# Optimization experiments

Hardware: AMD Instinct MI355X
Metric: run time of the kernel (lower is better)

Reference implementation:

```python
import jax, jax.numpy as jnp
import numpy as np


def segment_softmax(x, seg, num_segments):
    # numerically-stable softmax over graph segments (rows of the sparse matrix)
    m = jax.ops.segment_max(x, seg, num_segments=num_segments)
    e = jnp.exp(x - m[seg])
    s = jax.ops.segment_sum(e, seg, num_segments=num_segments)
    return e / s[seg]


def setup_inputs() -> dict:
    key = jax.random.key(0)
    ks = jax.random.split(key, 12)
    B, N, E, P, H = 256, 51200, 102400, 5, 300
    instruction = jax.random.normal(ks[0], (B, H), dtype=jnp.float32)
    distribution = jax.random.uniform(ks[1], (N,), dtype=jnp.float32)
    node_attrs = jax.random.normal(ks[2], (N, H), dtype=jnp.float32)
    edge_attrs = jax.random.normal(ks[3], (E, H), dtype=jnp.float32)
    node_indices = jnp.sort(jax.random.randint(ks[4], (N,), 0, B)).astype(jnp.int32)
    edge_batch_indices = jax.random.randint(ks[5], (E,), 0, B).astype(jnp.int32)
    edge_indices = jax.random.randint(ks[6], (2, E), 0, N).astype(jnp.int32)
    prop_embeds = jax.random.normal(ks[7], (P, H), dtype=jnp.float32)
    Ws_property = jax.random.uniform(ks[8], (P, H, H), dtype=jnp.float32)
    W_state = jax.random.uniform(ks[9], (H,), dtype=jnp.float32)
    W_relation = jax.random.uniform(ks[10], (H,), dtype=jnp.float32)
    return {"instruction": instruction, "distribution": distribution, "node_attrs": node_attrs,
            "edge_attrs": edge_attrs, "node_indices": node_indices,
            "edge_batch_indices": edge_batch_indices, "edge_indices": edge_indices,
            "prop_embeds": prop_embeds, "Ws_property": Ws_property,
            "W_state": W_state, "W_relation": W_relation}


def reference(instruction, distribution, node_attrs, edge_attrs, node_indices,
              edge_batch_indices, edge_indices, prop_embeds, Ws_property,
              W_state, W_relation):
    B = instruction.shape[0]
    # [B, P] property similarities
    prop_sim = jax.nn.softmax(instruction @ prop_embeds.T, axis=1)
    ps_node = prop_sim[node_indices]            # [N, P]
    instr_node = instruction[node_indices]      # [N, H]
    # per-property transform of node attrs: [N, P-1, H]
    wx = jnp.einsum('phk,nk->nph', Ws_property[:-1], node_attrs)
    node_scores = jax.nn.elu(jnp.sum(ps_node[:, :-1, None] * instr_node[:, None, :] * wx, axis=1))  # [N, H]
    # relation transform of edge attrs: [E, H]
    edge_wx = jnp.einsum('hk,ek->eh', Ws_property[-1], edge_attrs)
    edge_scores = jax.nn.elu(instruction[edge_batch_indices] * edge_wx)  # [E, H]
    # per-graph (segment) softmax over state logits
    state_logits = node_scores @ W_state        # [N]
    next_states = segment_softmax(state_logits, node_indices, B)
    # scatter-add message passing: dst node accumulates distribution[src] * edge_scores
    agg = jnp.zeros_like(node_scores).at[edge_indices[1]].add(
        distribution[edge_indices[0], None] * edge_scores)  # [N, H]
    rel_logits = agg @ W_relation               # [N]
    next_relations = segment_softmax(rel_logits, node_indices, B)
    r = ps_node[:, -1]
    next_distribution = r * next_relations + (1.0 - r) * next_states
    return next_distribution, prop_sim
```

## Files before the change

kernel.cpp:

```cpp
#include <hip/hip_runtime.h>
#include <math.h>

#define H 300
#define PP 5
#define NE 128
#define KC 32
#define NCH 10
#define WROWS 320
#define ROWB 128
#define WTILE (WROWS * ROWB)
#define ATILE (NE * ROWB)
#define NTHREADS 256
#define GT 512

using short8 = __attribute__((ext_vector_type(8))) short;
using f32x4  = __attribute__((ext_vector_type(4))) float;

__device__ __forceinline__ float wsum64(float v) {
#pragma unroll
    for (int m = 32; m >= 1; m >>= 1) v += __shfl_xor(v, m, 64);
    return v;
}
__device__ __forceinline__ float wmax64(float v) {
#pragma unroll
    for (int m = 32; m >= 1; m >>= 1) v = fmaxf(v, __shfl_xor(v, m, 64));
    return v;
}
__device__ __forceinline__ float eluf(float x) { return x > 0.f ? x : expm1f(x); }

__device__ __forceinline__ unsigned short f2bf(float x) {
    unsigned int u = __float_as_uint(x);
    unsigned int r = u + 0x7FFF + ((u >> 16) & 1);
    return (unsigned short)(r >> 16);
}
__device__ __forceinline__ float bf2f(unsigned short h) {
    return __uint_as_float(((unsigned int)h) << 16);
}
__device__ __forceinline__ int sw(int r, int kb) {
    return r * ROWB + (kb ^ ((r & 7) << 4));
}
__device__ __forceinline__ void split4(const float* v, uint2& ph, uint2& pl) {
    unsigned short hs[4], ls[4];
#pragma unroll
    for (int i = 0; i < 4; ++i) {
        hs[i] = f2bf(v[i]);
        ls[i] = f2bf(v[i] - bf2f(hs[i]));
    }
    ph = make_uint2((unsigned)hs[0] | ((unsigned)hs[1] << 16),
                    (unsigned)hs[2] | ((unsigned)hs[3] << 16));
    pl = make_uint2((unsigned)ls[0] | ((unsigned)ls[1] << 16),
                    (unsigned)ls[2] | ((unsigned)ls[3] << 16));
}
__device__ __forceinline__ void gload16(const void* g, void* lds) {
    __builtin_amdgcn_global_load_lds(
        (const __attribute__((address_space(1))) unsigned int*)g,
        (__attribute__((address_space(3))) unsigned int*)lds, 16, 0, 0);
}
#define SBAR() __builtin_amdgcn_s_barrier()
#define SCHED() __builtin_amdgcn_sched_barrier(0)
#define WAIT_LGKM() asm volatile("s_waitcnt lgkmcnt(0)" ::: "memory")
#define WAIT_VM2()  asm volatile("s_waitcnt vmcnt(2) lgkmcnt(0)" ::: "memory")
#define WAIT_VM0()  asm volatile("s_waitcnt vmcnt(0) lgkmcnt(0)" ::: "memory")

__global__ void k_prop_sim(const float* __restrict__ instr,
                           const float* __restrict__ pe,
                           float* __restrict__ prop_sim) {
    int b = blockIdx.x, lane = threadIdx.x;
    float dots[PP];
#pragma unroll
    for (int p = 0; p < PP; ++p) {
        float s = 0.f;
        for (int hh = lane; hh < H; hh += 64) s += instr[b * H + hh] * pe[p * H + hh];
        dots[p] = wsum64(s);
    }
    if (lane == 0) {
        float m = dots[0];
#pragma unroll
        for (int p = 1; p < PP; ++p) m = fmaxf(m, dots[p]);
        float e[PP], s = 0.f;
#pragma unroll
        for (int p = 0; p < PP; ++p) { e[p] = expf(dots[p] - m); s += e[p]; }
        float inv = 1.f / s;
#pragma unroll
        for (int p = 0; p < PP; ++p) prop_sim[b * PP + p] = e[p] * inv;
    }
}

__global__ void k_counts(const int* __restrict__ idx, int* __restrict__ counts, int N) {
    int i = blockIdx.x * blockDim.x + threadIdx.x;
    if (i < N) atomicAdd(&counts[idx[i]], 1);
}

__global__ void k_scan(const int* __restrict__ counts, int* __restrict__ offsets, int B) {
    __shared__ int sh[256];
    int t = threadIdx.x;
    int c = (t < B) ? counts[t] : 0;
    sh[t] = c;
    __syncthreads();
    for (int off = 1; off < 256; off <<= 1) {
        int v = (t >= off) ? sh[t - off] : 0;
        __syncthreads();
        sh[t] += v;
        __syncthreads();
    }
    if (t < B) offsets[t] = sh[t] - c;
    if (t == B - 1) offsets[B] = sh[t];
}

__global__ void k_presplit(const float* __restrict__ W4, char* __restrict__ img) {
    int c = blockIdx.x;
    int idx = blockIdx.y * NTHREADS + threadIdx.x;
    int r = idx >> 3, j = idx & 7;
    int k = c * KC + j * 4;
    float v[4] = {0.f, 0.f, 0.f, 0.f};
    if (r < H && k < H) *(float4*)v = *(const float4*)&W4[(size_t)r * H + k];
    uint2 ph, pl;
    split4(v, ph, pl);
    char* row = img + (size_t)c * WTILE + (size_t)r * ROWB;
    int x = (r & 7) << 4;
    *(uint2*)(row + ((j * 8) ^ x)) = ph;
    *(uint2*)(row + ((64 + j * 8) ^ x)) = pl;
}

__global__ void k_combine(const float* __restrict__ Ws,
                          const float* __restrict__ prop_sim,
                          char* __restrict__ img) {
    int b = blockIdx.x, c = blockIdx.y, t = threadIdx.x;
    float ps0 = prop_sim[b * PP + 0], ps1 = prop_sim[b * PP + 1];
    float ps2 = prop_sim[b * PP + 2], ps3 = prop_sim[b * PP + 3];
    char* tile = img + ((size_t)b * NCH + c) * WTILE;
#pragma unroll
    for (int i = 0; i < 10; ++i) {
        int idx = t + i * NTHREADS;
        int r = idx >> 3, j = idx & 7;
        int k = c * KC + j * 4;
        float cv[4] = {0.f, 0.f, 0.f, 0.f};
        if (r < H && k < H) {
            size_t base = (size_t)r * H + k;
            float w0[4], w1[4], w2[4], w3[4];
            *(float4*)w0 = *(const float4*)&Ws[0 * (size_t)H * H + base];
            *(float4*)w1 = *(const float4*)&Ws[1 * (size_t)H * H + base];
            *(float4*)w2 = *(const float4*)&Ws[2 * (size_t)H * H + base];
            *(float4*)w3 = *(const float4*)&Ws[3 * (size_t)H * H + base];
#pragma unroll
            for (int q = 0; q < 4; ++q)
                cv[q] = fmaf(ps0, w0[q], fmaf(ps1, w1[q], fmaf(ps2, w2[q], ps3 * w3[q])));
        }
        uint2 ph, pl;
        split4(cv, ph, pl);
        char* row = tile + (size_t)r * ROWB;
        int x = (r & 7) << 4;
        *(uint2*)(row + ((j * 8) ^ x)) = ph;
        *(uint2*)(row + ((64 + j * 8) ^ x)) = pl;
    }
}

__global__ __launch_bounds__(GT, 2) void k_gemm(
    const float* __restrict__ na, const float* __restrict__ ea,
    const char* __restrict__ Wc_img, const char* __restrict__ Wr_img,
    const float* __restrict__ instr, const float* __restrict__ wstate,
    const float* __restrict__ wrel,
    const int* __restrict__ offsets, const int* __restrict__ eb,
    const int* __restrict__ ei, const float* __restrict__ dist,
    float* __restrict__ slog, float* __restrict__ rlog,
    int N, int E, int nodeBlks)
{
    __shared__ __align__(16) char W_t[WTILE];
    __shared__ __align__(16) char A_t[ATILE];

    int bid = blockIdx.x;
    bool isNode = bid < nodeBlks;
    const float* Asrc;
    const char* Wsrc;
    int base, rowmax, b = 0, nn = NE;
    if (isNode) {
        int low3 = bid & 7, q = bid >> 3;
        int tile = q % 3, bhi = q / 3;
        b = bhi * 8 + low3;
        int start = offsets[b], end = offsets[b + 1];
        base = start + tile * NE;
        if (base >= end) return;
        nn = min(NE, end - base);
        rowmax = N - 1;
        Asrc = na;
        Wsrc = Wc_img + (size_t)b * NCH * WTILE;
    } else {
        base = (bid - nodeBlks) * NE;
        rowmax = E - 1;
        Asrc = ea;
        Wsrc = Wr_img;
    }

    int t = threadIdx.x;
    int w = t >> 6, l = t & 63, lane16 = l & 15, g = l >> 4;
    int wn = w & 3, wh = w >> 2;

    f32x4 acc[10][2];
#pragma unroll
    for (int ht = 0; ht < 10; ++ht)
#pragma unroll
        for (int cg = 0; cg < 2; ++cg) acc[ht][cg] = (f32x4){0.f, 0.f, 0.f, 0.f};

    float4 pa[2];
    auto loadA = [&](int c) {
#pragma unroll
        for (int i = 0; i < 2; ++i) {
            int idx = t + i * GT;
            int r = idx >> 3, j = idx & 7;
            int k = c * KC + j * 4;
            float4 v = {0.f, 0.f, 0.f, 0.f};
            if (k < H) {
                int row = min(base + r, rowmax);
                v = *(const float4*)&Asrc[(size_t)row * H + k];
            }
            pa[i] = v;
        }
    };
    auto storeA = [&]() {
#pragma unroll
        for (int i = 0; i < 2; ++i) {
            int idx = t + i * GT;
            int r = idx >> 3, j = idx & 7;
            float v[4] = {pa[i].x, pa[i].y, pa[i].z, pa[i].w};
            uint2 ph, pl;
            split4(v, ph, pl);
            *(uint2*)(A_t + sw(r, j * 8)) = ph;
            *(uint2*)(A_t + sw(r, 64 + j * 8)) = pl;
        }
    };
    auto gloadW = [&](int c) {
        const char* src = Wsrc + (size_t)c * WTILE;
        int goff = w * 5120 + (t & 63) * 16;
        int loff = w * 5120;
#pragma unroll
        for (int s = 0; s < 5; ++s)
            gload16(src + s * 1024 + goff, W_t + s * 1024 + loff);
    };

    loadA(0);
    storeA();
    gloadW(0);
    SCHED();
    loadA(1);
    SCHED();
    WAIT_VM2();
    SBAR();
    SCHED();

    for (int c = 0; c < NCH; ++c) {
        short8 bh[2], bl[2];
#pragma unroll
        for (int cg = 0; cg < 2; ++cg) {
            int brow = wn * 32 + cg * 16 + lane16;
            bh[cg] = *(const short8*)(A_t + sw(brow, g * 16));
            bl[cg] = *(const short8*)(A_t + sw(brow, 64 + g * 16));
        }
#pragma unroll
        for (int ht = 0; ht < 10; ++ht) {
            int arow = (wh * 10 + ht) * 16 + lane16;
            short8 ah = *(const short8*)(W_t + sw(arow, g * 16));
            short8 al = *(const short8*)(W_t + sw(arow, 64 + g * 16));
#pragma unroll
            for (int cg = 0; cg < 2; ++cg) {
                acc[ht][cg] = __builtin_amdgcn_mfma_f32_16x16x32_bf16(ah, bh[cg], acc[ht][cg], 0, 0, 0);
                acc[ht][cg] = __builtin_amdgcn_mfma_f32_16x16x32_bf16(ah, bl[cg], acc[ht][cg], 0, 0, 0);
                acc[ht][cg] = __builtin_amdgcn_mfma_f32_16x16x32_bf16(al, bh[cg], acc[ht][cg], 0, 0, 0);
            }
        }
        if (c + 1 < NCH) {
            WAIT_LGKM();
            SBAR();
            SCHED();
            storeA();
            gloadW(c + 1);
            SCHED();
            if (c + 2 < NCH) {
                loadA(c + 2);
                SCHED();
                WAIT_VM2();
            } else {
                WAIT_VM0();
            }
            SBAR();
            SCHED();
        }
    }

    if (isNode) {
        const float* insb = instr + (size_t)b * H;
#pragma unroll
        for (int cg = 0; cg < 2; ++cg) {
            float part = 0.f;
#pragma unroll
            for (int ht = 0; ht < 10; ++ht) {
                int hb = wh * 160 + ht * 16 + g * 4;
#pragma unroll
                for (int r = 0; r < 4; ++r) {
                    int h = hb + r;
                    if (h < H) part += wstate[h] * eluf(insb[h] * acc[ht][cg][r]);
                }
            }
            part += __shfl_xor(part, 16, 64);
            part += __shfl_xor(part, 32, 64);
            int col = wn * 32 + cg * 16 + lane16;
            if (l < 16 && col < nn) atomicAdd(&slog[base + col], part);
        }
    } else {
#pragma unroll
        for (int cg = 0; cg < 2; ++cg) {
            int e = base + wn * 32 + cg * 16 + lane16;
            int be = eb[e];
            const float* insb = instr + (size_t)be * H;
            float part = 0.f;
#pragma unroll
            for (int ht = 0; ht < 10; ++ht) {
                int hb = wh * 160 + ht * 16 + g * 4;
#pragma unroll
                for (int r = 0; r < 4; ++r) {
                    int h = hb + r;
                    if (h < H) part += wrel[h] * eluf(insb[h] * acc[ht][cg][r]);
                }
            }
            part += __shfl_xor(part, 16, 64);
            part += __shfl_xor(part, 32, 64);
            if (l < 16) atomicAdd(&rlog[ei[E + e]], dist[ei[e]] * part);
        }
    }
}

__global__ void k_final(const float* __restrict__ slog, const float* __restrict__ rlog,
                        const float* __restrict__ prop_sim, const int* __restrict__ offsets,
                        float* __restrict__ out)
{
    int b = blockIdx.x;
    int s0 = offsets[b], e1 = offsets[b + 1];
    int t = threadIdx.x, wave = t >> 6, lane = t & 63;
    __shared__ float shA[4], shB[4];
    float mS = -3.0e38f, mR = -3.0e38f;
    for (int i = s0 + t; i < e1; i += 256) {
        mS = fmaxf(mS, slog[i]);
        mR = fmaxf(mR, rlog[i]);
    }
    mS = wmax64(mS); mR = wmax64(mR);
    if (lane == 0) { shA[wave] = mS; shB[wave] = mR; }
    __syncthreads();
    mS = fmaxf(fmaxf(shA[0], shA[1]), fmaxf(shA[2], shA[3]));
    mR = fmaxf(fmaxf(shB[0], shB[1]), fmaxf(shB[2], shB[3]));
    __syncthreads();
    float sS = 0.f, sR = 0.f;
    for (int i = s0 + t; i < e1; i += 256) {
        sS += expf(slog[i] - mS);
        sR += expf(rlog[i] - mR);
    }
    sS = wsum64(sS); sR = wsum64(sR);
    if (lane == 0) { shA[wave] = sS; shB[wave] = sR; }
    __syncthreads();
    sS = shA[0] + shA[1] + shA[2] + shA[3];
    sR = shB[0] + shB[1] + shB[2] + shB[3];
    float r = prop_sim[b * PP + (PP - 1)];
    float iS = 1.f / sS, iR = 1.f / sR;
    for (int i = s0 + t; i < e1; i += 256) {
        float ns = expf(slog[i] - mS) * iS;
        float nr = expf(rlog[i] - mR) * iR;
        out[i] = r * nr + (1.f - r) * ns;
    }
}

extern "C" void kernel_launch(void* const* d_in, const int* in_sizes, int n_in,
                              void* d_out, int out_size, void* d_ws, size_t ws_size,
                              hipStream_t stream) {
    (void)n_in; (void)out_size; (void)ws_size;
    const float* instruction  = (const float*)d_in[0];
    const float* distribution = (const float*)d_in[1];
    const float* node_attrs   = (const float*)d_in[2];
    const float* edge_attrs   = (const float*)d_in[3];
    const int*   node_indices = (const int*)d_in[4];
    const int*   edge_batch   = (const int*)d_in[5];
    const int*   edge_indices = (const int*)d_in[6];
    const float* prop_embeds  = (const float*)d_in[7];
    const float* Ws           = (const float*)d_in[8];
    const float* W_state      = (const float*)d_in[9];
    const float* W_rel        = (const float*)d_in[10];

    int B = in_sizes[0] / H;
    int N = in_sizes[1];
    int E = in_sizes[5];

    float* out = (float*)d_out;
    float* prop_sim = out + N;

    float* ws = (float*)d_ws;
    float* state_logits = ws;
    float* rel_logits   = ws + N;
    int*   offsets      = (int*)(ws + 2 * (size_t)N);
    int*   counts       = offsets + (B + 1);
    uintptr_t wsp = (uintptr_t)(counts + B);
    wsp = (wsp + 255) & ~(uintptr_t)255;
    char* Wr_img = (char*)wsp;
    char* Wc_img = Wr_img + (size_t)NCH * WTILE;

    size_t zero_bytes = (size_t)2 * N * sizeof(float) + (size_t)(2 * B + 1) * sizeof(int);
    hipMemsetAsync(d_ws, 0, zero_bytes, stream);

    int nodeBlks = 3 * B;
    int edgeBlks = E / NE;

    k_prop_sim<<<B, 64, 0, stream>>>(instruction, prop_embeds, prop_sim);
    k_presplit<<<dim3(NCH, 10), NTHREADS, 0, stream>>>(Ws + 4 * (size_t)H * H, Wr_img);
    k_counts<<<(N + 255) / 256, 256, 0, stream>>>(node_indices, counts, N);
    k_scan<<<1, 256, 0, stream>>>(counts, offsets, B);
    k_combine<<<dim3(B, NCH), NTHREADS, 0, stream>>>(Ws, prop_sim, Wc_img);
    k_gemm<<<nodeBlks + edgeBlks, GT, 0, stream>>>(
        node_attrs, edge_attrs, Wc_img, Wr_img, instruction, W_state, W_rel,
        offsets, edge_batch, edge_indices, distribution,
        state_logits, rel_logits, N, E, nodeBlks);
    k_final<<<B, 256, 0, stream>>>(state_logits, rel_logits, prop_sim, offsets, out);
}
```

Before: 367.5 us.

## Rebalance wave tiling to 4x2 and stage W through registers instead of direct LDS loads

Each wave now covers 80 output rows by 64 columns (5x4 MFMA tiles) instead of 160x32, so each A fragment read from LDS feeds more MFMAs and fewer W fragment reads are needed per chunk. The W tile is no longer loaded with global_load_lds; it is prefetched into registers and written to LDS alongside the A tile, and the wait before the barrier becomes an lgkmcnt wait. This trades LDS read traffic and the direct-to-LDS path for extra VGPR pressure and explicit register staging of W, which could lower occupancy.

```diff
diff --git a/kernel.cpp b/kernel.cpp
--- a/kernel.cpp
+++ b/kernel.cpp
@@ -51,16 +51,9 @@
     pl = make_uint2((unsigned)ls[0] | ((unsigned)ls[1] << 16),
                     (unsigned)ls[2] | ((unsigned)ls[3] << 16));
 }
-__device__ __forceinline__ void gload16(const void* g, void* lds) {
-    __builtin_amdgcn_global_load_lds(
-        (const __attribute__((address_space(1))) unsigned int*)g,
-        (__attribute__((address_space(3))) unsigned int*)lds, 16, 0, 0);
-}
 #define SBAR() __builtin_amdgcn_s_barrier()
 #define SCHED() __builtin_amdgcn_sched_barrier(0)
 #define WAIT_LGKM() asm volatile("s_waitcnt lgkmcnt(0)" ::: "memory")
-#define WAIT_VM2()  asm volatile("s_waitcnt vmcnt(2) lgkmcnt(0)" ::: "memory")
-#define WAIT_VM0()  asm volatile("s_waitcnt vmcnt(0) lgkmcnt(0)" ::: "memory")
 
 __global__ void k_prop_sim(const float* __restrict__ instr,
                            const float* __restrict__ pe,
@@ -193,15 +186,17 @@
 
     int t = threadIdx.x;
     int w = t >> 6, l = t & 63, lane16 = l & 15, g = l >> 4;
-    int wn = w & 3, wh = w >> 2;
-
-    f32x4 acc[10][2];
-#pragma unroll
-    for (int ht = 0; ht < 10; ++ht)
-#pragma unroll
-        for (int cg = 0; cg < 2; ++cg) acc[ht][cg] = (f32x4){0.f, 0.f, 0.f, 0.f};
+    int wn = w & 1, wh = w >> 1;
+
+    f32x4 acc[5][4];
+#pragma unroll
+    for (int ht = 0; ht < 5; ++ht)
+#pragma unroll
+        for (int cg = 0; cg < 4; ++cg) acc[ht][cg] = (f32x4){0.f, 0.f, 0.f, 0.f};
 
     float4 pa[2];
+    uint4  pw[5];
+
     auto loadA = [&](int c) {
 #pragma unroll
         for (int i = 0; i < 2; ++i) {
@@ -228,40 +223,42 @@
             *(uint2*)(A_t + sw(r, 64 + j * 8)) = pl;
         }
     };
-    auto gloadW = [&](int c) {
-        const char* src = Wsrc + (size_t)c * WTILE;
-        int goff = w * 5120 + (t & 63) * 16;
-        int loff = w * 5120;
+    auto loadW = [&](int c) {
+        const char* src = Wsrc + (size_t)c * WTILE + t * 16;
 #pragma unroll
         for (int s = 0; s < 5; ++s)
-            gload16(src + s * 1024 + goff, W_t + s * 1024 + loff);
+            pw[s] = *(const uint4*)(src + s * 8192);
     };
-
-    loadA(0);
-    storeA();
-    gloadW(0);
+    auto storeW = [&]() {
+        char* dst = W_t + t * 16;
+#pragma unroll
+        for (int s = 0; s < 5; ++s)
+            *(uint4*)(dst + s * 8192) = pw[s];
+    };
+
+    loadA(0); loadW(0);
+    storeA(); storeW();
+    loadA(1); loadW(1);
     SCHED();
-    loadA(1);
-    SCHED();
-    WAIT_VM2();
+    WAIT_LGKM();
     SBAR();
     SCHED();
 
     for (int c = 0; c < NCH; ++c) {
-        short8 bh[2], bl[2];
-#pragma unroll
-        for (int cg = 0; cg < 2; ++cg) {
-            int brow = wn * 32 + cg * 16 + lane16;
+        short8 bh[4], bl[4];
+#pragma unroll
+        for (int cg = 0; cg < 4; ++cg) {
+            int brow = wn * 64 + cg * 16 + lane16;
             bh[cg] = *(const short8*)(A_t + sw(brow, g * 16));
             bl[cg] = *(const short8*)(A_t + sw(brow, 64 + g * 16));
         }
 #pragma unroll
-        for (int ht = 0; ht < 10; ++ht) {
-            int arow = (wh * 10 + ht) * 16 + lane16;
+        for (int ht = 0; ht < 5; ++ht) {
+            int arow = wh * 80 + ht * 16 + lane16;
             short8 ah = *(const short8*)(W_t + sw(arow, g * 16));
             short8 al = *(const short8*)(W_t + sw(arow, 64 + g * 16));
 #pragma unroll
-            for (int cg = 0; cg < 2; ++cg) {
+            for (int cg = 0; cg < 4; ++cg) {
                 acc[ht][cg] = __builtin_amdgcn_mfma_f32_16x16x32_bf16(ah, bh[cg], acc[ht][cg], 0, 0, 0);
                 acc[ht][cg] = __builtin_amdgcn_mfma_f32_16x16x32_bf16(ah, bl[cg], acc[ht][cg], 0, 0, 0);
                 acc[ht][cg] = __builtin_amdgcn_mfma_f32_16x16x32_bf16(al, bh[cg], acc[ht][cg], 0, 0, 0);
@@ -271,16 +268,10 @@
             WAIT_LGKM();
             SBAR();
             SCHED();
-            storeA();
-            gloadW(c + 1);
+            storeA(); storeW();
+            if (c + 2 < NCH) { loadA(c + 2); loadW(c + 2); }
             SCHED();
-            if (c + 2 < NCH) {
-                loadA(c + 2);
-                SCHED();
-                WAIT_VM2();
-            } else {
-                WAIT_VM0();
-            }
+            WAIT_LGKM();
             SBAR();
             SCHED();
         }
@@ -289,11 +280,11 @@
     if (isNode) {
         const float* insb = instr + (size_t)b * H;
 #pragma unroll
-        for (int cg = 0; cg < 2; ++cg) {
+        for (int cg = 0; cg < 4; ++cg) {
             float part = 0.f;
 #pragma unroll
-            for (int ht = 0; ht < 10; ++ht) {
-                int hb = wh * 160 + ht * 16 + g * 4;
+            for (int ht = 0; ht < 5; ++ht) {
+                int hb = wh * 80 + ht * 16 + g * 4;
 #pragma unroll
                 for (int r = 0; r < 4; ++r) {
                     int h = hb + r;
@@ -302,19 +293,19 @@
             }
             part += __shfl_xor(part, 16, 64);
             part += __shfl_xor(part, 32, 64);
-            int col = wn * 32 + cg * 16 + lane16;
+            int col = wn * 64 + cg * 16 + lane16;
             if (l < 16 && col < nn) atomicAdd(&slog[base + col], part);
         }
     } else {
 #pragma unroll
-        for (int cg = 0; cg < 2; ++cg) {
-            int e = base + wn * 32 + cg * 16 + lane16;
+        for (int cg = 0; cg < 4; ++cg) {
+            int e = base + wn * 64 + cg * 16 + lane16;
             int be = eb[e];
             const float* insb = instr + (size_t)be * H;
             float part = 0.f;
 #pragma unroll
-            for (int ht = 0; ht < 10; ++ht) {
-                int hb = wh * 160 + ht * 16 + g * 4;
+            for (int ht = 0; ht < 5; ++ht) {
+                int hb = wh * 80 + ht * 16 + g * 4;
 #pragma unroll
                 for (int r = 0; r < 4; ++r) {
                     int h = hb + r;
```

After: 517.1 us. 1.41x slower.

## Split GEMM output rows across two grid halves and double-buffer weight tiles

Applied to the files above, without the earlier changes.

The GEMM grid gains a second dimension that splits the 320 output rows into two halves of 160, so each block holds half the accumulators and loads half the weight tile per chunk. The freed LDS holds two half-tiles, which lets weight loads be prefetched two chunks ahead, and the waits are rewritten with per-wave vmcnt values to match. The intent is to cut register pressure, add more blocks for occupancy, and hide weight-load latency. The cost is that every activation tile is loaded, split to bf16 and stored twice, and the atomics on the logits double.

```diff
diff --git a/kernel.cpp b/kernel.cpp
--- a/kernel.cpp
+++ b/kernel.cpp
@@ -6,9 +6,9 @@
 #define NE 128
 #define KC 32
 #define NCH 10
-#define WROWS 320
 #define ROWB 128
-#define WTILE (WROWS * ROWB)
+#define WTILE (320 * ROWB)
+#define WHALF (160 * ROWB)
 #define ATILE (NE * ROWB)
 #define NTHREADS 256
 #define GT 512
@@ -59,8 +59,9 @@
 #define SBAR() __builtin_amdgcn_s_barrier()
 #define SCHED() __builtin_amdgcn_sched_barrier(0)
 #define WAIT_LGKM() asm volatile("s_waitcnt lgkmcnt(0)" ::: "memory")
-#define WAIT_VM2()  asm volatile("s_waitcnt vmcnt(2) lgkmcnt(0)" ::: "memory")
-#define WAIT_VM0()  asm volatile("s_waitcnt vmcnt(0) lgkmcnt(0)" ::: "memory")
+#define WAIT_VM0()  asm volatile("s_waitcnt vmcnt(0)" ::: "memory")
+#define WAIT_VM4()  asm volatile("s_waitcnt vmcnt(4)" ::: "memory")
+#define WAIT_VM5()  asm volatile("s_waitcnt vmcnt(5)" ::: "memory")
 
 __global__ void k_prop_sim(const float* __restrict__ instr,
                            const float* __restrict__ pe,
@@ -165,10 +166,11 @@
     float* __restrict__ slog, float* __restrict__ rlog,
     int N, int E, int nodeBlks)
 {
-    __shared__ __align__(16) char W_t[WTILE];
+    __shared__ __align__(16) char W_t[2][WHALF];
     __shared__ __align__(16) char A_t[ATILE];
 
     int bid = blockIdx.x;
+    int hz = blockIdx.y;
     bool isNode = bid < nodeBlks;
     const float* Asrc;
     const char* Wsrc;
@@ -183,25 +185,26 @@
         nn = min(NE, end - base);
         rowmax = N - 1;
         Asrc = na;
-        Wsrc = Wc_img + (size_t)b * NCH * WTILE;
+        Wsrc = Wc_img + (size_t)b * NCH * WTILE + (size_t)hz * WHALF;
     } else {
         base = (bid - nodeBlks) * NE;
         rowmax = E - 1;
         Asrc = ea;
-        Wsrc = Wr_img;
+        Wsrc = Wr_img + (size_t)hz * WHALF;
     }
 
     int t = threadIdx.x;
     int w = t >> 6, l = t & 63, lane16 = l & 15, g = l >> 4;
     int wn = w & 3, wh = w >> 2;
 
-    f32x4 acc[10][2];
-#pragma unroll
-    for (int ht = 0; ht < 10; ++ht)
+    f32x4 acc[5][2];
+#pragma unroll
+    for (int ht = 0; ht < 5; ++ht)
 #pragma unroll
         for (int cg = 0; cg < 2; ++cg) acc[ht][cg] = (f32x4){0.f, 0.f, 0.f, 0.f};
 
     float4 pa[2];
+
     auto loadA = [&](int c) {
 #pragma unroll
         for (int i = 0; i < 2; ++i) {
@@ -228,25 +231,27 @@
             *(uint2*)(A_t + sw(r, 64 + j * 8)) = pl;
         }
     };
-    auto gloadW = [&](int c) {
+    auto gloadW = [&](int c, int sel) {
         const char* src = Wsrc + (size_t)c * WTILE;
-        int goff = w * 5120 + (t & 63) * 16;
-        int loff = w * 5120;
-#pragma unroll
-        for (int s = 0; s < 5; ++s)
-            gload16(src + s * 1024 + goff, W_t + s * 1024 + loff);
+        char* dst = W_t[sel];
+        int off = w * 1024 + (l << 4);
+        gload16(src + off, dst + off);
+        gload16(src + 8192 + off, dst + 8192 + off);
+        if (w < 4) gload16(src + 16384 + off, dst + 16384 + off);
     };
 
     loadA(0);
+    gloadW(0, 0);
     storeA();
-    gloadW(0);
+    loadA(1);
+    gloadW(1, 1);
     SCHED();
-    loadA(1);
-    SCHED();
-    WAIT_VM2();
+    if (w < 4) { WAIT_VM5(); } else { WAIT_VM4(); }
+    WAIT_LGKM();
     SBAR();
     SCHED();
 
+    int curb = 0;
     for (int c = 0; c < NCH; ++c) {
         short8 bh[2], bl[2];
 #pragma unroll
@@ -256,10 +261,10 @@
             bl[cg] = *(const short8*)(A_t + sw(brow, 64 + g * 16));
         }
 #pragma unroll
-        for (int ht = 0; ht < 10; ++ht) {
-            int arow = (wh * 10 + ht) * 16 + lane16;
-            short8 ah = *(const short8*)(W_t + sw(arow, g * 16));
-            short8 al = *(const short8*)(W_t + sw(arow, 64 + g * 16));
+        for (int ht = 0; ht < 5; ++ht) {
+            int arow = wh * 80 + ht * 16 + lane16;
+            short8 ah = *(const short8*)(W_t[curb] + sw(arow, g * 16));
+            short8 al = *(const short8*)(W_t[curb] + sw(arow, 64 + g * 16));
 #pragma unroll
             for (int cg = 0; cg < 2; ++cg) {
                 acc[ht][cg] = __builtin_amdgcn_mfma_f32_16x16x32_bf16(ah, bh[cg], acc[ht][cg], 0, 0, 0);
@@ -272,17 +277,19 @@
             SBAR();
             SCHED();
             storeA();
-            gloadW(c + 1);
-            SCHED();
             if (c + 2 < NCH) {
                 loadA(c + 2);
+                gloadW(c + 2, curb);
                 SCHED();
-                WAIT_VM2();
+                if (w < 4) { WAIT_VM5(); } else { WAIT_VM4(); }
             } else {
+                SCHED();
                 WAIT_VM0();
             }
+            WAIT_LGKM();
             SBAR();
             SCHED();
+            curb ^= 1;
         }
     }
 
@@ -292,8 +299,8 @@
         for (int cg = 0; cg < 2; ++cg) {
             float part = 0.f;
 #pragma unroll
-            for (int ht = 0; ht < 10; ++ht) {
-                int hb = wh * 160 + ht * 16 + g * 4;
+            for (int ht = 0; ht < 5; ++ht) {
+                int hb = hz * 160 + wh * 80 + ht * 16 + g * 4;
 #pragma unroll
                 for (int r = 0; r < 4; ++r) {
                     int h = hb + r;
@@ -313,8 +320,8 @@
             const float* insb = instr + (size_t)be * H;
             float part = 0.f;
 #pragma unroll
-            for (int ht = 0; ht < 10; ++ht) {
-                int hb = wh * 160 + ht * 16 + g * 4;
+            for (int ht = 0; ht < 5; ++ht) {
+                int hb = hz * 160 + wh * 80 + ht * 16 + g * 4;
 #pragma unroll
                 for (int r = 0; r < 4; ++r) {
                     int h = hb + r;
@@ -410,7 +417,7 @@
     k_counts<<<(N + 255) / 256, 256, 0, stream>>>(node_indices, counts, N);
     k_scan<<<1, 256, 0, stream>>>(counts, offsets, B);
     k_combine<<<dim3(B, NCH), NTHREADS, 0, stream>>>(Ws, prop_sim, Wc_img);
-    k_gemm<<<nodeBlks + edgeBlks, GT, 0, stream>>>(
+    k_gemm<<<dim3(nodeBlks + edgeBlks, 2), GT, 0, stream>>>(
         node_attrs, edge_attrs, Wc_img, Wr_img, instruction, W_state, W_rel,
         offsets, edge_batch, edge_indices, distribution,
         state_logits, rel_logits, N, E, nodeBlks);
```

Result: faster. 337.9 us (-8.1%).
